# Optimization experiments

Measured on AMD Instinct MI355X. Metric: run time of the kernel, lower is better.

## Reference

```python
import jax, jax.numpy as jnp
import numpy as np

N_ROOMS = 126          # len(building.rooms)
N = 2 + N_ROOMS        # state dim (reset_iv: 2 + n_rooms)
M = 1 + N_ROOMS        # input dim u = [Tout, Q_watts...]
T = 200000             # number of eval times
DT = 30.0              # seconds between eval points
TOUT_DT = 3600.0       # outside-temp table grid spacing (s)
K = 1700               # table length (covers 1000 + T*DT seconds)
LOAD_MAX = 500.0       # physical_loads_scaling: W/m^2 upper bound


def setup_inputs() -> dict:
    key = jax.random.key(0)
    ks = jax.random.split(key, 6)
    # Stable RC-style state matrix: negative diagonal dominates
    A = 1e-5 * jax.random.normal(ks[0], (N, N), dtype=jnp.float32) - 2e-4 * jnp.eye(N, dtype=jnp.float32)
    B = 1e-6 * jax.random.normal(ks[1], (N, M), dtype=jnp.float32)
    loads = jax.random.normal(ks[2], (2, N_ROOMS), dtype=jnp.float32)   # raw params (pre-sigmoid)
    areas = 10.0 + 40.0 * jax.random.uniform(ks[3], (N_ROOMS,), dtype=jnp.float32)  # room areas m^2
    Tout_vals = 10.0 + 5.0 * jax.random.normal(ks[4], (K,), dtype=jnp.float32)      # hourly Tout table
    t_eval = 1000.0 + DT * jnp.arange(T, dtype=jnp.float32)
    iv = 26.0 * jnp.ones((N, 1), dtype=jnp.float32)
    return {"A": A, "B": B, "loads": loads, "areas": areas,
            "Tout_vals": Tout_vals, "t_eval": t_eval, "iv": iv, "action": 1}


def _interp_tout(vals, t):
    # linear interpolation on a uniform grid starting at t=0 (replaces scipy interp1d)
    pos = t / TOUT_DT
    idx = jnp.clip(jnp.floor(pos).astype(jnp.int32), 0, K - 2)
    w = pos - idx.astype(pos.dtype)
    return vals[idx] * (1.0 - w) + vals[idx + 1] * w


def reference(A, B, loads, areas, Tout_vals, t_eval, iv, action):
    t0 = t_eval[0]
    ts = t_eval - t0
    # _build_loads: sigmoid transform + physical scaling
    lp = jax.nn.sigmoid(loads) * LOAD_MAX
    cool_load, gain_load = lp[0], lp[1]
    # f_ode constants: Q_area = -cool*action + gain; Q_watts = proportional_heating
    Q_watts = (-cool_load * action + gain_load) * areas        # [n_rooms]
    b_q = B[:, 1:] @ Q_watts                                   # [N] constant forcing
    b_T = B[:, 0]                                              # [N] Tout coupling
    x0 = iv[:, 0]

    def f(t, x):
        Tout = _interp_tout(Tout_vals, t + t0)
        return A @ x + b_T * Tout + b_q

    # torchdiffeq method='rk4' -> rk4_alt_step_func (3/8 rule)
    def step(x, tt):
        t, tn = tt
        dt = tn - t
        k1 = f(t, x)
        k2 = f(t + dt / 3.0, x + dt * k1 / 3.0)
        k3 = f(t + dt * 2.0 / 3.0, x + dt * (k2 - k1 / 3.0))
        k4 = f(t + dt, x + dt * (k1 - k2 + k3))
        xn = x + dt * (k1 + 3.0 * (k2 + k3) + k4) / 8.0
        return xn, xn

    _, traj = jax.lax.scan(step, x0, (ts[:-1], ts[1:]))
    out = jnp.concatenate([x0[None, :], traj], axis=0)         # [T, N]
    return out[..., None]                                      # [T, N, 1] matching iv shape
```

## Files before the change

kernel.cpp:

```cpp
#include <hip/hip_runtime.h>

#define N 128
#define NR 126
#define MBCOL 127
#define TSTEPS 200000
#define L1 49
#define C1 4096
#define KT 1700

#define OFF_Z     0
#define OFF_S     16384
#define OFF_P     32768
#define OFF_PW2   65536
#define OFF_PW4   81920
#define OFF_PW8   98304
#define OFF_PW16  114688
#define OFF_PW32  131072
#define OFF_Q     147456
#define OFF_WC    180224
#define OFF_ACC   212992
#define OFF_DELTA 737280
#define OFF_B1    753664
#define OFF_B2    1015808
#define OFF_B3    1146880
#define OFF_A16   1212416
#define OFF_C1    1245184
#define OFF_C2    1261568
#define OFF_C3    1269760
#define OFF_A256  1273856
#define OFF_BQ256 1275904
#define OFF_BST16 753664
#define OFF_Q256  786432

typedef float v4f __attribute__((ext_vector_type(4)));
typedef __attribute__((ext_vector_type(8))) short bf16x8;
typedef __attribute__((ext_vector_type(4))) float f32x4;

#define OFF_PEH   65536
#define OFF_PEL   75776

#define LBAR() do { \
  __builtin_amdgcn_sched_barrier(0); \
  asm volatile("s_waitcnt lgkmcnt(0)" ::: "memory"); \
  __builtin_amdgcn_sched_barrier(0); \
  __builtin_amdgcn_s_barrier(); \
  __builtin_amdgcn_sched_barrier(0); \
} while (0)

#define GLD4(dst, p) \
  asm volatile("global_load_dwordx4 %0, %1, off" : "=v"(dst) : "v"(p))
#define PINQ(q) \
  asm volatile("s_waitcnt vmcnt(0)" \
    : "+v"(q[0]),"+v"(q[1]),"+v"(q[2]),"+v"(q[3]), \
      "+v"(q[4]),"+v"(q[5]),"+v"(q[6]),"+v"(q[7]), \
      "+v"(q[8]),"+v"(q[9]),"+v"(q[10]),"+v"(q[11]), \
      "+v"(q[12]),"+v"(q[13]),"+v"(q[14]),"+v"(q[15]))
#define PINQ8(q) \
  asm volatile("s_waitcnt vmcnt(0)" \
    : "+v"(q[0]),"+v"(q[1]),"+v"(q[2]),"+v"(q[3]), \
      "+v"(q[4]),"+v"(q[5]),"+v"(q[6]),"+v"(q[7]))

__device__ __forceinline__ void loadQ16(v4f* qv, const float* pb)
{
  #pragma unroll
  for (int s = 0; s < 16; ++s) GLD4(qv[s], pb + 4*s);
  PINQ(qv);
}

__device__ __forceinline__ void bsplit(float f, unsigned short& h, unsigned short& l)
{
  unsigned int u = __float_as_uint(f);
  unsigned int r = (u + 0x7FFFu + ((u >> 16) & 1u)) >> 16;
  float hf = __uint_as_float(r << 16);
  h = (unsigned short)r;
  float lo = f - hf;
  unsigned int u2 = __float_as_uint(lo);
  unsigned int r2 = (u2 + 0x7FFFu + ((u2 >> 16) & 1u)) >> 16;
  l = (unsigned short)r2;
}

__global__ __launch_bounds__(128) void kPrep(
    const float* __restrict__ A, const float* __restrict__ B,
    const float* __restrict__ loads, const float* __restrict__ areas,
    const float* __restrict__ iv, const int* __restrict__ action,
    float* __restrict__ ws, float* __restrict__ out)
{
  __shared__ float qw[NR];
  __shared__ float ys[4][N];
  __shared__ float qs[4][N];
  int t = threadIdx.x;
  float actf = (float)action[0];
  if (t < NR) {
    float lc = (1.0f / (1.0f + expf(-loads[t]))) * 500.0f;
    float lg = (1.0f / (1.0f + expf(-loads[NR + t]))) * 500.0f;
    qw[t] = (-lc * actf + lg) * areas[t];
  }
  __syncthreads();
  {
    float bq = 0.0f;
    for (int i = 0; i < NR; ++i) bq += B[t * MBCOL + 1 + i] * qw[i];
    ys[0][t] = B[t * MBCOL];
    qs[0][t] = bq;
  }
  __syncthreads();
  for (int s = 1; s < 4; ++s) {
    float ay = 0.0f, aq = 0.0f;
    for (int k = 0; k < N; ++k) {
      float a = A[t * N + k];
      ay += a * ys[s-1][k];
      aq += a * qs[s-1][k];
    }
    ys[s][t] = 30.0f * ay;
    qs[s][t] = 30.0f * aq;
    __syncthreads();
  }
  float vs[5];
  vs[0] = 3.75f * (ys[0][t] + ys[1][t] + ys[2][t]*(1.0f/3.0f) + ys[3][t]*(1.0f/3.0f));
  vs[1] = 3.75f * (3.0f*ys[0][t] + 2.0f*ys[1][t] + ys[2][t]);
  vs[2] = 3.75f * (3.0f*ys[0][t] + ys[1][t]);
  vs[3] = 3.75f * ys[0][t];
  vs[4] = 3.75f * (8.0f*qs[0][t] + 4.0f*qs[1][t] + (4.0f/3.0f)*qs[2][t] + (1.0f/3.0f)*qs[3][t]);
  for (int m = 0; m < 5; ++m) ws[OFF_WC + (m*L1) * N + t] = vs[m];
  for (int i = t; i < N*N/4; i += 128) {
    float4 a = ((const float4*)A)[i];
    a.x *= 30.0f; a.y *= 30.0f; a.z *= 30.0f; a.w *= 30.0f;
    ((float4*)(ws + OFF_Z))[i] = a;
  }
  out[t] = iv[t];
}

__device__ __forceinline__ void mmRowR(const float* __restrict__ Aw,
                                       const float* __restrict__ Bw,
                                       float* __restrict__ Cw,
                                       float* __restrict__ Cw2,
                                       float* __restrict__ sm, int r)
{
  int t = threadIdx.x, c = t & 127, kh = t >> 7;
  const float* Ar = Aw + r*N + kh*64;
  const float* Bc = Bw + (kh*64)*N + c;
  float p0=0.f, p1=0.f, p2=0.f, p3=0.f;
  #pragma unroll 4
  for (int s = 0; s < 64; s += 4) {
    const float4 av = *(const float4*)(Ar + s);
    p0 = fmaf(av.x, Bc[(s+0)*N], p0);
    p1 = fmaf(av.y, Bc[(s+1)*N], p1);
    p2 = fmaf(av.z, Bc[(s+2)*N], p2);
    p3 = fmaf(av.w, Bc[(s+3)*N], p3);
  }
  sm[kh*128 + c] = (p0+p1)+(p2+p3);
  __syncthreads();
  if (kh == 0) {
    float v = sm[c] + sm[128 + c];
    Cw[r*N + c] = v;
    if (Cw2) Cw2[r*N + c] = v;
  }
}

__device__ __forceinline__ void polyRow(float* __restrict__ ws,
                                        float* __restrict__ sm)
{
  int t = threadIdx.x, c = t & 127, kh = t >> 7;
  int r = blockIdx.x;
  const float* Z = ws + OFF_Z;
  const float* S = ws + OFF_S;
  const float* Sr = S + r*N + kh*64;
  float x3=0.f, x4=0.f;
  #pragma unroll 4
  for (int s = 0; s < 64; s += 4) {
    const float4 av = *(const float4*)(Sr + s);
    int k = kh*64 + s;
    x3 = fmaf(av.x, Z[(k+0)*N+c], x3); x3 = fmaf(av.y, Z[(k+1)*N+c], x3);
    x3 = fmaf(av.z, Z[(k+2)*N+c], x3); x3 = fmaf(av.w, Z[(k+3)*N+c], x3);
    x4 = fmaf(av.x, S[(k+0)*N+c], x4); x4 = fmaf(av.y, S[(k+1)*N+c], x4);
    x4 = fmaf(av.z, S[(k+2)*N+c], x4); x4 = fmaf(av.w, S[(k+3)*N+c], x4);
  }
  sm[kh*128 + c] = x3;
  sm[256 + kh*128 + c] = x4;
  __syncthreads();
  if (kh == 0) {
    float a3 = sm[c] + sm[128+c];
    float a4 = sm[256+c] + sm[384+c];
    float pv = (r==c ? 1.0f : 0.0f) + Z[r*N+c] + 0.5f*S[r*N+c]
             + (1.0f/6.0f)*a3 + (1.0f/24.0f)*a4;
    ws[OFF_P + r*N + c] = pv;
  }
}

__device__ __forceinline__ void wUnit(const float* __restrict__ Pw,
                                      float* __restrict__ ws,
                                      int uw, int wbase, int wcount,
                                      float* __restrict__ wbuf )
{
  int t = threadIdx.x;
  int np = 5 * wcount;
  for (int i = t; i < 8*N; i += 256) {
    int pl = i >> 7, k = i & 127;
    int p = uw*8 + pl;
    float v = 0.0f;
    if (p < np) {
      int m = p / wcount, kk = p % wcount;
      v = ws[OFF_WC + (m*L1 + kk)*N + k];
    }
    wbuf[pl*N + k] = v;
  }
  __syncthreads();
  int r = t & 127, pg = t >> 7;
  float acc[4] = {0,0,0,0};
  #pragma unroll 2
  for (int k = 0; k < N; k += 4) {
    const float4 av = *(const float4*)(Pw + r*N + k);
    #pragma unroll
    for (int pi = 0; pi < 4; ++pi) {
      const float4 wv = *(const float4*)(wbuf + (pg*4+pi)*N + k);
      acc[pi] = fmaf(av.x, wv.x, acc[pi]);
      acc[pi] = fmaf(av.y, wv.y, acc[pi]);
      acc[pi] = fmaf(av.z, wv.z, acc[pi]);
      acc[pi] = fmaf(av.w, wv.w, acc[pi]);
    }
  }
  #pragma unroll
  for (int pi = 0; pi < 4; ++pi) {
    int p = uw*8 + pg*4 + pi;
    if (p < np) {
      int m = p / wcount, kk = p % wcount;
      ws[OFF_WC + (m*L1 + wbase + kk)*N + r] = acc[pi];
    }
  }
}

__device__ __forceinline__ void treeUnit(const float* __restrict__ Qm,
                                         const float* __restrict__ src,
                                         float* __restrict__ dst,
                                         int uw, float* __restrict__ wbuf)
{
  int t = threadIdx.x;
  for (int i = t; i < 8*N; i += 256) {
    int pl = i >> 7, k = i & 127;
    wbuf[pl*N + k] = src[(size_t)(2*(uw*8 + pl))*N + k];
  }
  __syncthreads();
  int r = t & 127, pg = t >> 7;
  float acc[4] = {0,0,0,0};
  #pragma unroll 2
  for (int k = 0; k < N; k += 4) {
    const float4 av = *(const float4*)(Qm + r*N + k);
    #pragma unroll
    for (int pi = 0; pi < 4; ++pi) {
      const float4 wv = *(const float4*)(wbuf + (pg*4+pi)*N + k);
      acc[pi] = fmaf(av.x, wv.x, acc[pi]);
      acc[pi] = fmaf(av.y, wv.y, acc[pi]);
      acc[pi] = fmaf(av.z, wv.z, acc[pi]);
      acc[pi] = fmaf(av.w, wv.w, acc[pi]);
    }
  }
  #pragma unroll
  for (int pi = 0; pi < 4; ++pi) {
    int j = uw*8 + pg*4 + pi;
    dst[(size_t)j*N + r] = acc[pi] + src[(size_t)(2*j + 1)*N + r];
  }
}

__global__ __launch_bounds__(256) void kPhase(float* __restrict__ ws, int ph)
{
  __shared__ float sm[1024];
  int b = blockIdx.x;
  if (ph >= 20) {
    int lv = ph - 20;
    const int srcO[8] = {OFF_ACC, OFF_B1, OFF_B2, OFF_B3, OFF_A16, OFF_C1, OFF_C2, OFF_C3};
    const int dstO[8] = {OFF_B1, OFF_B2, OFF_B3, OFF_A16, OFF_C1, OFF_C2, OFF_C3, OFF_A256};
    const int nco[8]  = {2048, 1024, 512, 256, 128, 64, 32, 16};
    const int qO[8]   = {OFF_Q, OFF_S, OFF_P, OFF_PW8, OFF_PW16, OFF_PW32, OFF_Z, OFF_DELTA};
    const int pS[8]   = {OFF_S, OFF_P, OFF_PW8, OFF_PW16, OFF_PW32, OFF_Z, OFF_DELTA, -1};
    const int pD[8]   = {OFF_P, OFF_PW8, OFF_PW16, OFF_PW32, OFF_Z, OFF_DELTA, OFF_Q256, -1};
    int nb = nco[lv] >> 3;
    if (b < nb) treeUnit(ws + qO[lv], ws + srcO[lv], ws + dstO[lv], b, sm);
    else if (pS[lv] >= 0) mmRowR(ws + pS[lv], ws + pS[lv], ws + pD[lv], nullptr, sm, b - nb);
    return;
  }
  if (ph == 1) { mmRowR(ws+OFF_Z, ws+OFF_Z, ws+OFF_S, nullptr, sm, b); return; }
  if (ph == 2) { polyRow(ws, sm); return; }
  if (ph <= 8) {
    int s = ph - 3;
    const int srcOff[6] = {OFF_P, OFF_PW2, OFF_PW4, OFF_PW8, OFF_PW16, OFF_PW32};
    const int dstOff[6] = {OFF_PW2, OFF_PW4, OFF_PW8, OFF_PW16, OFF_PW32, OFF_S};
    if (b < 128) {
      if (s < 5) mmRowR(ws+srcOff[s], ws+srcOff[s], ws+dstOff[s], nullptr, sm, b);
      else       mmRowR(ws+OFF_PW32, ws+OFF_PW16, ws+OFF_S, nullptr, sm, b);
    } else {
      int wbase  = (s < 5) ? (1 << s) : 32;
      int wcount = (s < 5) ? (1 << s) : 17;
      wUnit(ws + srcOff[s], ws, b - 128, wbase, wcount, sm);
    }
    return;
  }
  if (ph == 9) {
    if (b < 128) {
      mmRowR(ws+OFF_S, ws+OFF_P, ws+OFF_Z, ws+OFF_Q, sm, b);
    } else {
      int r = b - 128;
      int tt = threadIdx.x;
      if (tt < 160) {
        float val;
        if (tt < 128)      val = ws[OFF_P + r*N + tt];
        else if (tt < 133) val = ws[OFF_WC + ((tt-128)*L1)*N + r];
        else               val = 0.0f;
        unsigned short h, l2;
        bsplit(val, h, l2);
        ((unsigned short*)(ws + OFF_PEH))[r*160 + tt] = h;
        ((unsigned short*)(ws + OFF_PEL))[r*160 + tt] = l2;
      }
    }
    return;
  }
}

__device__ __forceinline__ void build_table(float* lt, const float* __restrict__ Tout,
                                            int J0, int t, int cnt, int stride)
{
  int tbase = 1470*J0 + 1000;
  for (int s = t; s < cnt; s += stride) {
    float tt = (float)(tbase + 10*s);
    float pos = tt / 3600.0f;
    int idx = (int)pos;
    if (idx > KT-2) idx = KT-2;
    float w = pos - (float)idx;
    lt[s] = Tout[idx]*(1.0f-w) + Tout[idx+1]*w;
  }
}

__global__ __launch_bounds__(256) void k3_acc(const float* __restrict__ Tout,
                                              float* __restrict__ ws)
{
  __shared__ float lt[1184];
  int t = threadIdx.x;
  if (blockIdx.x >= 512) {
    mmRowR(ws+OFF_Z, ws+OFF_Z, ws+OFF_S, nullptr, lt, blockIdx.x - 512);
    return;
  }
  int J0 = blockIdx.x * 8;
  build_table(lt, Tout, J0, t, 1177, 256);
  __syncthreads();
  int r = t & 127, jh = t >> 7;
  float a[4] = {0.0f, 0.0f, 0.0f, 0.0f};
  for (int k = 0; k < L1; ++k) {
    float w0 = ws[OFF_WC + (0*L1+k)*N + r];
    float w1 = ws[OFF_WC + (1*L1+k)*N + r];
    float w2 = ws[OFF_WC + (2*L1+k)*N + r];
    float w3 = ws[OFF_WC + (3*L1+k)*N + r];
    float w4 = ws[OFF_WC + (4*L1+k)*N + r];
    #pragma unroll
    for (int q = 0; q < 4; ++q) {
      int cl = jh*4 + q;
      int soff = 3*(L1*cl + (L1-1) - k);
      a[q] += w0*lt[soff] + w1*lt[soff+1] + w2*lt[soff+2] + w3*lt[soff+3] + w4;
    }
  }
  #pragma unroll
  for (int q = 0; q < 4; ++q)
    ws[OFF_ACC + (size_t)(J0 + jh*4 + q)*N + r] = a[q];
}

__device__ __forceinline__ void mv_step3(const v4f* qv, float* x, float* ps,
                                         int r, int kh, float addv)
{
  const v4f* xp = (const v4f*)(x + kh*64);
  float p0=0.f, p1=0.f, p2=0.f, p3=0.f;
  #pragma unroll
  for (int s = 0; s < 16; s += 4) {
    v4f x0 = xp[s+0], x1 = xp[s+1], x2 = xp[s+2], x3 = xp[s+3];
    p0 = fmaf(qv[s+0][0],x0[0],p0); p0 = fmaf(qv[s+0][1],x0[1],p0);
    p0 = fmaf(qv[s+0][2],x0[2],p0); p0 = fmaf(qv[s+0][3],x0[3],p0);
    p1 = fmaf(qv[s+1][0],x1[0],p1); p1 = fmaf(qv[s+1][1],x1[1],p1);
    p1 = fmaf(qv[s+1][2],x1[2],p1); p1 = fmaf(qv[s+1][3],x1[3],p1);
    p2 = fmaf(qv[s+2][0],x2[0],p2); p2 = fmaf(qv[s+2][1],x2[1],p2);
    p2 = fmaf(qv[s+2][2],x2[2],p2); p2 = fmaf(qv[s+2][3],x2[3],p2);
    p3 = fmaf(qv[s+3][0],x3[0],p3); p3 = fmaf(qv[s+3][1],x3[1],p3);
    p3 = fmaf(qv[s+3][2],x3[2],p3); p3 = fmaf(qv[s+3][3],x3[3],p3);
  }
  ps[kh*128 + r] = (p0+p1)+(p2+p3);
  LBAR();
  if (kh == 0) x[r] = ps[r] + ps[128 + r] + addv;
  LBAR();
}

__global__ __launch_bounds__(256, 2) void k5a_l3(const float* __restrict__ iv,
                                                 float* __restrict__ ws)
{
  __shared__ float x[N];
  __shared__ float ps[256];
  __shared__ float dl[15*N];
  int t = threadIdx.x, r = t & 127, kh = t >> 7;
  v4f qv[16];
  loadQ16(qv, ws + OFF_Q256 + r*N + kh*64);
  for (int i = t; i < 15*N; i += 256) dl[i] = ws[OFF_A256 + i];
  if (t < N) x[t] = iv[t];
  __syncthreads();
  for (int p = 0; p < 16; ++p) {
    if (kh == 0) ws[OFF_BQ256 + p*N + r] = x[r];
    if (p == 15) break;
    mv_step3(qv, x, ps, r, kh, dl[p*N + r]);
  }
}

__global__ __launch_bounds__(256, 2) void k5b_l2(float* __restrict__ ws)
{
  __shared__ float x[N];
  __shared__ float ps[256];
  __shared__ float dl[15*N];
  int t = threadIdx.x, r = t & 127, kh = t >> 7;
  int p = blockIdx.x;
  v4f qv[16];
  loadQ16(qv, ws + OFF_PW16 + r*N + kh*64);
  for (int i = t; i < 15*N; i += 256) dl[i] = ws[OFF_A16 + (size_t)p*15*0 + (size_t)(p*16)*N + i];
  if (t < N) x[t] = ws[OFF_BQ256 + p*N + t];
  __syncthreads();
  for (int i = 0; i < 16; ++i) {
    if (kh == 0) ws[OFF_BST16 + (size_t)(p*16 + i)*N + r] = x[r];
    if (i == 15) break;
    mv_step3(qv, x, ps, r, kh, dl[i*N + r]);
  }
}

__global__ __launch_bounds__(512) void k7_main(const float* __restrict__ Tout,
                                               const float* __restrict__ ws,
                                               float* __restrict__ out)
{
  __shared__ float ltp[3136];
  __shared__ __align__(16) unsigned short XbHi[16][168];
  __shared__ __align__(16) unsigned short XbLo[16][168];
  __shared__ float xf[N];
  __shared__ float psf[512];
  int t = threadIdx.x;
  int m = blockIdx.x;
  int J0 = m * 16;

  for (int e = t; e < 3136; e += 512) {
    int cl = e / 196, rem = e - cl*196;
    int i = rem >> 2, mm = rem & 3;
    float tt = (float)(1000 + 1470*(J0 + cl) + 30*i + 10*mm);
    float pos = tt / 3600.0f;
    int idx = (int)pos;
    if (idx > KT-2) idx = KT-2;
    float w = pos - (float)idx;
    ltp[e] = Tout[idx]*(1.0f-w) + Tout[idx+1]*w;
  }
  for (int e = t; e < 16*40; e += 512) {
    int cn = e / 40, k = 128 + (e - cn*40);
    XbHi[cn][k] = 0; XbLo[cn][k] = 0;
  }
  __syncthreads();
  if (t < 80) {
    int cn = t / 5, mm = t - cn*5;
    float v = (mm < 4) ? ltp[cn*196 + mm] : 1.0f;
    unsigned short h, l2; bsplit(v, h, l2);
    XbHi[cn][128+mm] = h; XbLo[cn][128+mm] = l2;
  }

  int r = t & 127, kq = t >> 7;
  v4f q8[8];
  #pragma unroll
  for (int s = 0; s < 8; ++s) GLD4(q8[s], ws + OFF_Q + r*N + kq*32 + 4*s);
  PINQ8(q8);
  if (t < N) xf[t] = ws[OFF_BST16 + (size_t)m*N + t];
  __syncthreads();
  float nxtA = (t < N) ? ws[OFF_ACC + (size_t)(J0)*N + t] : 0.0f;
  for (int c = 0; c < 16; ++c) {
    if (t < N) {
      unsigned short h, l2; bsplit(xf[t], h, l2);
      XbHi[c][t] = h; XbLo[c][t] = l2;
    }
    if (c == 15) { LBAR(); break; }
    float pp0 = 0.f, pp1 = 0.f;
    const v4f* xp = (const v4f*)(xf + kq*32);
    #pragma unroll
    for (int s = 0; s < 8; s += 2) {
      v4f x0 = xp[s], x1 = xp[s+1];
      pp0 = fmaf(q8[s][0],x0[0],pp0);   pp0 = fmaf(q8[s][1],x0[1],pp0);
      pp0 = fmaf(q8[s][2],x0[2],pp0);   pp0 = fmaf(q8[s][3],x0[3],pp0);
      pp1 = fmaf(q8[s+1][0],x1[0],pp1); pp1 = fmaf(q8[s+1][1],x1[1],pp1);
      pp1 = fmaf(q8[s+1][2],x1[2],pp1); pp1 = fmaf(q8[s+1][3],x1[3],pp1);
    }
    psf[t] = pp0 + pp1;
    LBAR();
    if (t < N) {
      float addv = nxtA;
      nxtA = ws[OFF_ACC + (size_t)(J0 + c + 1)*N + t];
      xf[t] = psf[t] + psf[t+128] + psf[t+256] + psf[t+384] + addv;
    }
    LBAR();
  }

  int l = t & 63, w = t >> 6;
  int la = l & 15, lg = l >> 4;
  int rowA = w*16 + la;
  const unsigned short* peh = (const unsigned short*)(ws + OFF_PEH);
  const unsigned short* pel = (const unsigned short*)(ws + OFF_PEL);
  bf16x8 Ah[5], Al[5];
  #pragma unroll
  for (int kt = 0; kt < 5; ++kt) {
    Ah[kt] = *(const bf16x8*)(peh + rowA*160 + kt*32 + lg*8);
    Al[kt] = *(const bf16x8*)(pel + rowA*160 + kt*32 + lg*8);
  }

  int rowD = w*16 + lg*4;
  int nnB = L1*(J0 + la);
  for (int i = 0; i < L1; ++i) {
    bf16x8 Bh[5], Bl[5];
    #pragma unroll
    for (int kt = 0; kt < 5; ++kt) {
      Bh[kt] = *(const bf16x8*)(&XbHi[la][kt*32 + lg*8]);
      Bl[kt] = *(const bf16x8*)(&XbLo[la][kt*32 + lg*8]);
    }
    f32x4 ahh = {0.f,0.f,0.f,0.f}, ahl = {0.f,0.f,0.f,0.f}, alh = {0.f,0.f,0.f,0.f};
    #pragma unroll
    for (int kt = 0; kt < 5; ++kt) {
      ahh = __builtin_amdgcn_mfma_f32_16x16x32_bf16(Ah[kt], Bh[kt], ahh, 0, 0, 0);
      ahl = __builtin_amdgcn_mfma_f32_16x16x32_bf16(Ah[kt], Bl[kt], ahl, 0, 0, 0);
      alh = __builtin_amdgcn_mfma_f32_16x16x32_bf16(Al[kt], Bh[kt], alh, 0, 0, 0);
    }
    f32x4 y = ahh + ahl + alh;
    int nn = nnB + i + 1;
    if (nn < TSTEPS)
      *(f32x4*)(out + (size_t)nn*N + rowD) = y;
    LBAR();
    unsigned short h0,h1,h2,h3,q0,q1,q2,q3;
    bsplit(y[0],h0,q0); bsplit(y[1],h1,q1); bsplit(y[2],h2,q2); bsplit(y[3],h3,q3);
    unsigned int hA = (unsigned)h0 | ((unsigned)h1<<16);
    unsigned int hB = (unsigned)h2 | ((unsigned)h3<<16);
    unsigned int lA = (unsigned)q0 | ((unsigned)q1<<16);
    unsigned int lB = (unsigned)q2 | ((unsigned)q3<<16);
    *reinterpret_cast<uint2*>(&XbHi[la][rowD]) = make_uint2(hA, hB);
    *reinterpret_cast<uint2*>(&XbLo[la][rowD]) = make_uint2(lA, lB);
    if (t < 64 && i < L1-1) {
      int cn = t >> 2, mm = t & 3;
      float v = ltp[cn*196 + (i+1)*4 + mm];
      unsigned short hh, ll; bsplit(v, hh, ll);
      XbHi[cn][128+mm] = hh; XbLo[cn][128+mm] = ll;
    }
    LBAR();
  }
}

extern "C" void kernel_launch(void* const* d_in, const int* in_sizes, int n_in,
                              void* d_out, int out_size, void* d_ws, size_t ws_size,
                              hipStream_t stream)
{
  const float* A     = (const float*)d_in[0];
  const float* B     = (const float*)d_in[1];
  const float* loads = (const float*)d_in[2];
  const float* areas = (const float*)d_in[3];
  const float* Tout  = (const float*)d_in[4];
  const float* iv    = (const float*)d_in[6];
  const int* action  = (const int*)d_in[7];
  float* out = (float*)d_out;
  float* ws  = (float*)d_ws;

  hipLaunchKernelGGL(kPrep, dim3(1), dim3(128), 0, stream,
                     A, B, loads, areas, iv, action, ws, out);
  const int phGrid[10] = {0, 128, 128, 129, 130, 131, 133, 138, 139, 256};
  for (int ph = 1; ph <= 9; ++ph)
    hipLaunchKernelGGL(kPhase, dim3(phGrid[ph]), dim3(256), 0, stream, ws, ph);
  hipLaunchKernelGGL(k3_acc, dim3(640), dim3(256), 0, stream, Tout, ws);
  const int trGrid[8] = {384, 256, 192, 160, 144, 136, 132, 2};
  for (int lv = 0; lv < 8; ++lv)
    hipLaunchKernelGGL(kPhase, dim3(trGrid[lv]), dim3(256), 0, stream, ws, 20 + lv);
  hipLaunchKernelGGL(k5a_l3, dim3(1),   dim3(256), 0, stream, iv, ws);
  hipLaunchKernelGGL(k5b_l2, dim3(16),  dim3(256), 0, stream, ws);
  hipLaunchKernelGGL(k7_main, dim3(256), dim3(512), 0, stream, Tout, ws, out);
}
```

Baseline: 228.4 us.

## Fold prep and final tree level into other kernels, double-buffer MFMA operand tiles

Removes the separate single-block prep kernel by computing A·A scaled directly from the input A and running the prep work in an extra block of phase 1. The last tree level and the two level-scan kernels are merged into one 16-block kernel, where each block redundantly recomputes the prefix it needs. This cuts the serial launch count by three. The main loop double-buffers the bf16 state tiles in LDS, which removes one barrier per step at the cost of more shared memory and some redundant per-block work in k5ab.

After: 216.3 us. 5.3% less time.

```diff
diff --git a/kernel.cpp b/kernel.cpp
--- a/kernel.cpp
+++ b/kernel.cpp
@@ -27,8 +27,6 @@
 #define OFF_C1    1245184
 #define OFF_C2    1261568
 #define OFF_C3    1269760
-#define OFF_A256  1273856
-#define OFF_BQ256 1275904
 #define OFF_BST16 753664
 #define OFF_Q256  786432
 
@@ -79,61 +77,11 @@
   l = (unsigned short)r2;
 }
 
-__global__ __launch_bounds__(128) void kPrep(
-    const float* __restrict__ A, const float* __restrict__ B,
-    const float* __restrict__ loads, const float* __restrict__ areas,
-    const float* __restrict__ iv, const int* __restrict__ action,
-    float* __restrict__ ws, float* __restrict__ out)
-{
-  __shared__ float qw[NR];
-  __shared__ float ys[4][N];
-  __shared__ float qs[4][N];
-  int t = threadIdx.x;
-  float actf = (float)action[0];
-  if (t < NR) {
-    float lc = (1.0f / (1.0f + expf(-loads[t]))) * 500.0f;
-    float lg = (1.0f / (1.0f + expf(-loads[NR + t]))) * 500.0f;
-    qw[t] = (-lc * actf + lg) * areas[t];
-  }
-  __syncthreads();
-  {
-    float bq = 0.0f;
-    for (int i = 0; i < NR; ++i) bq += B[t * MBCOL + 1 + i] * qw[i];
-    ys[0][t] = B[t * MBCOL];
-    qs[0][t] = bq;
-  }
-  __syncthreads();
-  for (int s = 1; s < 4; ++s) {
-    float ay = 0.0f, aq = 0.0f;
-    for (int k = 0; k < N; ++k) {
-      float a = A[t * N + k];
-      ay += a * ys[s-1][k];
-      aq += a * qs[s-1][k];
-    }
-    ys[s][t] = 30.0f * ay;
-    qs[s][t] = 30.0f * aq;
-    __syncthreads();
-  }
-  float vs[5];
-  vs[0] = 3.75f * (ys[0][t] + ys[1][t] + ys[2][t]*(1.0f/3.0f) + ys[3][t]*(1.0f/3.0f));
-  vs[1] = 3.75f * (3.0f*ys[0][t] + 2.0f*ys[1][t] + ys[2][t]);
-  vs[2] = 3.75f * (3.0f*ys[0][t] + ys[1][t]);
-  vs[3] = 3.75f * ys[0][t];
-  vs[4] = 3.75f * (8.0f*qs[0][t] + 4.0f*qs[1][t] + (4.0f/3.0f)*qs[2][t] + (1.0f/3.0f)*qs[3][t]);
-  for (int m = 0; m < 5; ++m) ws[OFF_WC + (m*L1) * N + t] = vs[m];
-  for (int i = t; i < N*N/4; i += 128) {
-    float4 a = ((const float4*)A)[i];
-    a.x *= 30.0f; a.y *= 30.0f; a.z *= 30.0f; a.w *= 30.0f;
-    ((float4*)(ws + OFF_Z))[i] = a;
-  }
-  out[t] = iv[t];
-}
-
-__device__ __forceinline__ void mmRowR(const float* __restrict__ Aw,
+__device__ __forceinline__ void mmRowS(const float* __restrict__ Aw,
                                        const float* __restrict__ Bw,
                                        float* __restrict__ Cw,
                                        float* __restrict__ Cw2,
-                                       float* __restrict__ sm, int r)
+                                       float* __restrict__ sm, int r, float scale)
 {
   int t = threadIdx.x, c = t & 127, kh = t >> 7;
   const float* Ar = Aw + r*N + kh*64;
@@ -150,18 +98,69 @@
   sm[kh*128 + c] = (p0+p1)+(p2+p3);
   __syncthreads();
   if (kh == 0) {
-    float v = sm[c] + sm[128 + c];
+    float v = (sm[c] + sm[128 + c]) * scale;
     Cw[r*N + c] = v;
     if (Cw2) Cw2[r*N + c] = v;
   }
 }
 
-__device__ __forceinline__ void polyRow(float* __restrict__ ws,
-                                        float* __restrict__ sm)
+#define mmRowR(Aw,Bw,Cw,Cw2,sm,r) mmRowS(Aw,Bw,Cw,Cw2,sm,r,1.0f)
+
+__device__ void prepLite(const float* __restrict__ A, const float* __restrict__ B,
+                         const float* __restrict__ loads, const float* __restrict__ areas,
+                         const float* __restrict__ iv, const int* __restrict__ action,
+                         float* __restrict__ ws, float* __restrict__ out,
+                         float* __restrict__ sm)
+{
+  float* qw = sm;
+  float* ys = sm + 128;
+  float* qs = sm + 640;
+  int t = threadIdx.x;
+  float actf = (float)action[0];
+  if (t < NR) {
+    float lc = (1.0f / (1.0f + expf(-loads[t]))) * 500.0f;
+    float lg = (1.0f / (1.0f + expf(-loads[NR + t]))) * 500.0f;
+    qw[t] = (-lc * actf + lg) * areas[t];
+  }
+  __syncthreads();
+  if (t < N) {
+    float bq = 0.0f;
+    for (int i = 0; i < NR; ++i) bq += B[t * MBCOL + 1 + i] * qw[i];
+    ys[t] = B[t * MBCOL];
+    qs[t] = bq;
+  }
+  __syncthreads();
+  for (int s = 1; s < 4; ++s) {
+    if (t < N) {
+      float ay = 0.0f, aq = 0.0f;
+      for (int k = 0; k < N; ++k) {
+        float a = A[t * N + k];
+        ay += a * ys[(s-1)*N + k];
+        aq += a * qs[(s-1)*N + k];
+      }
+      ys[s*N + t] = 30.0f * ay;
+      qs[s*N + t] = 30.0f * aq;
+    }
+    __syncthreads();
+  }
+  if (t < N) {
+    float y0 = ys[t], y1 = ys[N+t], y2 = ys[2*N+t], y3 = ys[3*N+t];
+    float q0 = qs[t], q1 = qs[N+t], q2 = qs[2*N+t], q3 = qs[3*N+t];
+    ws[OFF_WC + (0*L1)*N + t] = 3.75f * (y0 + y1 + y2*(1.0f/3.0f) + y3*(1.0f/3.0f));
+    ws[OFF_WC + (1*L1)*N + t] = 3.75f * (3.0f*y0 + 2.0f*y1 + y2);
+    ws[OFF_WC + (2*L1)*N + t] = 3.75f * (3.0f*y0 + y1);
+    ws[OFF_WC + (3*L1)*N + t] = 3.75f * y0;
+    ws[OFF_WC + (4*L1)*N + t] = 3.75f * (8.0f*q0 + 4.0f*q1 + (4.0f/3.0f)*q2 + (1.0f/3.0f)*q3);
+    out[t] = iv[t];
+  }
+}
+
+__device__ __forceinline__ void polyRowA(const float* __restrict__ A,
+                                         float* __restrict__ ws,
+                                         float* __restrict__ sm)
 {
   int t = threadIdx.x, c = t & 127, kh = t >> 7;
   int r = blockIdx.x;
-  const float* Z = ws + OFF_Z;
   const float* S = ws + OFF_S;
   const float* Sr = S + r*N + kh*64;
   float x3=0.f, x4=0.f;
@@ -169,8 +168,8 @@
   for (int s = 0; s < 64; s += 4) {
     const float4 av = *(const float4*)(Sr + s);
     int k = kh*64 + s;
-    x3 = fmaf(av.x, Z[(k+0)*N+c], x3); x3 = fmaf(av.y, Z[(k+1)*N+c], x3);
-    x3 = fmaf(av.z, Z[(k+2)*N+c], x3); x3 = fmaf(av.w, Z[(k+3)*N+c], x3);
+    x3 = fmaf(av.x, A[(k+0)*N+c], x3); x3 = fmaf(av.y, A[(k+1)*N+c], x3);
+    x3 = fmaf(av.z, A[(k+2)*N+c], x3); x3 = fmaf(av.w, A[(k+3)*N+c], x3);
     x4 = fmaf(av.x, S[(k+0)*N+c], x4); x4 = fmaf(av.y, S[(k+1)*N+c], x4);
     x4 = fmaf(av.z, S[(k+2)*N+c], x4); x4 = fmaf(av.w, S[(k+3)*N+c], x4);
   }
@@ -178,9 +177,9 @@
   sm[256 + kh*128 + c] = x4;
   __syncthreads();
   if (kh == 0) {
-    float a3 = sm[c] + sm[128+c];
+    float a3 = 30.0f * (sm[c] + sm[128+c]);
     float a4 = sm[256+c] + sm[384+c];
-    float pv = (r==c ? 1.0f : 0.0f) + Z[r*N+c] + 0.5f*S[r*N+c]
+    float pv = (r==c ? 1.0f : 0.0f) + 30.0f*A[r*N+c] + 0.5f*S[r*N+c]
              + (1.0f/6.0f)*a3 + (1.0f/24.0f)*a4;
     ws[OFF_P + r*N + c] = pv;
   }
@@ -260,25 +259,33 @@
   }
 }
 
-__global__ __launch_bounds__(256) void kPhase(float* __restrict__ ws, int ph)
-{
-  __shared__ float sm[1024];
+__global__ __launch_bounds__(256) void kPhase(
+    const float* __restrict__ A, const float* __restrict__ B,
+    const float* __restrict__ loads, const float* __restrict__ areas,
+    const float* __restrict__ iv, const int* __restrict__ action,
+    float* __restrict__ ws, float* __restrict__ out, int ph)
+{
+  __shared__ float sm[1280];
   int b = blockIdx.x;
   if (ph >= 20) {
     int lv = ph - 20;
-    const int srcO[8] = {OFF_ACC, OFF_B1, OFF_B2, OFF_B3, OFF_A16, OFF_C1, OFF_C2, OFF_C3};
-    const int dstO[8] = {OFF_B1, OFF_B2, OFF_B3, OFF_A16, OFF_C1, OFF_C2, OFF_C3, OFF_A256};
-    const int nco[8]  = {2048, 1024, 512, 256, 128, 64, 32, 16};
-    const int qO[8]   = {OFF_Q, OFF_S, OFF_P, OFF_PW8, OFF_PW16, OFF_PW32, OFF_Z, OFF_DELTA};
-    const int pS[8]   = {OFF_S, OFF_P, OFF_PW8, OFF_PW16, OFF_PW32, OFF_Z, OFF_DELTA, -1};
-    const int pD[8]   = {OFF_P, OFF_PW8, OFF_PW16, OFF_PW32, OFF_Z, OFF_DELTA, OFF_Q256, -1};
+    const int srcO[7] = {OFF_ACC, OFF_B1, OFF_B2, OFF_B3, OFF_A16, OFF_C1, OFF_C2};
+    const int dstO[7] = {OFF_B1, OFF_B2, OFF_B3, OFF_A16, OFF_C1, OFF_C2, OFF_C3};
+    const int nco[7]  = {2048, 1024, 512, 256, 128, 64, 32};
+    const int qO[7]   = {OFF_Q, OFF_S, OFF_P, OFF_PW8, OFF_PW16, OFF_PW32, OFF_Z};
+    const int pS[7]   = {OFF_S, OFF_P, OFF_PW8, OFF_PW16, OFF_PW32, OFF_Z, OFF_DELTA};
+    const int pD[7]   = {OFF_P, OFF_PW8, OFF_PW16, OFF_PW32, OFF_Z, OFF_DELTA, OFF_Q256};
     int nb = nco[lv] >> 3;
     if (b < nb) treeUnit(ws + qO[lv], ws + srcO[lv], ws + dstO[lv], b, sm);
-    else if (pS[lv] >= 0) mmRowR(ws + pS[lv], ws + pS[lv], ws + pD[lv], nullptr, sm, b - nb);
+    else mmRowR(ws + pS[lv], ws + pS[lv], ws + pD[lv], nullptr, sm, b - nb);
     return;
   }
-  if (ph == 1) { mmRowR(ws+OFF_Z, ws+OFF_Z, ws+OFF_S, nullptr, sm, b); return; }
-  if (ph == 2) { polyRow(ws, sm); return; }
+  if (ph == 1) {
+    if (b < 128) mmRowS(A, A, ws+OFF_S, nullptr, sm, b, 900.0f);
+    else prepLite(A, B, loads, areas, iv, action, ws, out, sm);
+    return;
+  }
+  if (ph == 2) { polyRowA(A, ws, sm); return; }
   if (ph <= 8) {
     int s = ph - 3;
     const int srcOff[6] = {OFF_P, OFF_PW2, OFF_PW4, OFF_PW8, OFF_PW16, OFF_PW32};
@@ -383,41 +390,52 @@
   LBAR();
 }
 
-__global__ __launch_bounds__(256, 2) void k5a_l3(const float* __restrict__ iv,
-                                                 float* __restrict__ ws)
+__global__ __launch_bounds__(256, 2) void k5ab(const float* __restrict__ iv,
+                                               float* __restrict__ ws)
 {
   __shared__ float x[N];
   __shared__ float ps[256];
-  __shared__ float dl[15*N];
-  int t = threadIdx.x, r = t & 127, kh = t >> 7;
-  v4f qv[16];
-  loadQ16(qv, ws + OFF_Q256 + r*N + kh*64);
-  for (int i = t; i < 15*N; i += 256) dl[i] = ws[OFF_A256 + i];
-  if (t < N) x[t] = iv[t];
-  __syncthreads();
-  for (int p = 0; p < 16; ++p) {
-    if (kh == 0) ws[OFF_BQ256 + p*N + r] = x[r];
-    if (p == 15) break;
-    mv_step3(qv, x, ps, r, kh, dl[p*N + r]);
-  }
-}
-
-__global__ __launch_bounds__(256, 2) void k5b_l2(float* __restrict__ ws)
-{
-  __shared__ float x[N];
-  __shared__ float ps[256];
-  __shared__ float dl[15*N];
+  __shared__ float c3[32*N];
+  __shared__ float aq[15*N];
+  __shared__ float a16d[15*N];
   int t = threadIdx.x, r = t & 127, kh = t >> 7;
   int p = blockIdx.x;
+  for (int i = t; i < 32*N; i += 256) c3[i] = ws[OFF_C3 + i];
+  for (int i = t; i < 15*N; i += 256) a16d[i] = ws[OFF_A16 + (size_t)(p*16)*N + i];
+  if (t < N) x[t] = iv[t];
   v4f qv[16];
+  loadQ16(qv, ws + OFF_DELTA + r*N + kh*64);
+  __syncthreads();
+  for (int q = 0; q < p; ++q) {
+    const v4f* xp = (const v4f*)(c3 + (size_t)(2*q)*N + kh*64);
+    float p0=0.f, p1=0.f, p2=0.f, p3=0.f;
+    #pragma unroll
+    for (int s = 0; s < 16; s += 4) {
+      v4f x0 = xp[s+0], x1 = xp[s+1], x2 = xp[s+2], x3 = xp[s+3];
+      p0 = fmaf(qv[s+0][0],x0[0],p0); p0 = fmaf(qv[s+0][1],x0[1],p0);
+      p0 = fmaf(qv[s+0][2],x0[2],p0); p0 = fmaf(qv[s+0][3],x0[3],p0);
+      p1 = fmaf(qv[s+1][0],x1[0],p1); p1 = fmaf(qv[s+1][1],x1[1],p1);
+      p1 = fmaf(qv[s+1][2],x1[2],p1); p1 = fmaf(qv[s+1][3],x1[3],p1);
+      p2 = fmaf(qv[s+2][0],x2[0],p2); p2 = fmaf(qv[s+2][1],x2[1],p2);
+      p2 = fmaf(qv[s+2][2],x2[2],p2); p2 = fmaf(qv[s+2][3],x2[3],p2);
+      p3 = fmaf(qv[s+3][0],x3[0],p3); p3 = fmaf(qv[s+3][1],x3[1],p3);
+      p3 = fmaf(qv[s+3][2],x3[2],p3); p3 = fmaf(qv[s+3][3],x3[3],p3);
+    }
+    ps[kh*128 + r] = (p0+p1)+(p2+p3);
+    LBAR();
+    if (kh == 0) aq[q*N + r] = ps[r] + ps[128 + r] + c3[(size_t)(2*q+1)*N + r];
+    LBAR();
+  }
+  loadQ16(qv, ws + OFF_Q256 + r*N + kh*64);
+  __syncthreads();
+  for (int q = 0; q < p; ++q)
+    mv_step3(qv, x, ps, r, kh, aq[q*N + r]);
   loadQ16(qv, ws + OFF_PW16 + r*N + kh*64);
-  for (int i = t; i < 15*N; i += 256) dl[i] = ws[OFF_A16 + (size_t)p*15*0 + (size_t)(p*16)*N + i];
-  if (t < N) x[t] = ws[OFF_BQ256 + p*N + t];
   __syncthreads();
   for (int i = 0; i < 16; ++i) {
     if (kh == 0) ws[OFF_BST16 + (size_t)(p*16 + i)*N + r] = x[r];
     if (i == 15) break;
-    mv_step3(qv, x, ps, r, kh, dl[i*N + r]);
+    mv_step3(qv, x, ps, r, kh, a16d[i*N + r]);
   }
 }
 
@@ -426,8 +444,8 @@
                                                float* __restrict__ out)
 {
   __shared__ float ltp[3136];
-  __shared__ __align__(16) unsigned short XbHi[16][168];
-  __shared__ __align__(16) unsigned short XbLo[16][168];
+  __shared__ __align__(16) unsigned short XbHi[2][16][168];
+  __shared__ __align__(16) unsigned short XbLo[2][16][168];
   __shared__ float xf[N];
   __shared__ float psf[512];
   int t = threadIdx.x;
@@ -444,16 +462,17 @@
     float w = pos - (float)idx;
     ltp[e] = Tout[idx]*(1.0f-w) + Tout[idx+1]*w;
   }
-  for (int e = t; e < 16*40; e += 512) {
-    int cn = e / 40, k = 128 + (e - cn*40);
-    XbHi[cn][k] = 0; XbLo[cn][k] = 0;
+  for (int e = t; e < 2*16*40; e += 512) {
+    int bu = e / 640, rem = e - bu*640;
+    int cn = rem / 40, k = 128 + (rem - cn*40);
+    XbHi[bu][cn][k] = 0; XbLo[bu][cn][k] = 0;
   }
   __syncthreads();
   if (t < 80) {
     int cn = t / 5, mm = t - cn*5;
     float v = (mm < 4) ? ltp[cn*196 + mm] : 1.0f;
     unsigned short h, l2; bsplit(v, h, l2);
-    XbHi[cn][128+mm] = h; XbLo[cn][128+mm] = l2;
+    XbHi[0][cn][128+mm] = h; XbLo[0][cn][128+mm] = l2;
   }
 
   int r = t & 127, kq = t >> 7;
@@ -467,7 +486,7 @@
   for (int c = 0; c < 16; ++c) {
     if (t < N) {
       unsigned short h, l2; bsplit(xf[t], h, l2);
-      XbHi[c][t] = h; XbLo[c][t] = l2;
+      XbHi[0][c][t] = h; XbLo[0][c][t] = l2;
     }
     if (c == 15) { LBAR(); break; }
     float pp0 = 0.f, pp1 = 0.f;
@@ -505,11 +524,12 @@
   int rowD = w*16 + lg*4;
   int nnB = L1*(J0 + la);
   for (int i = 0; i < L1; ++i) {
+    int cur = i & 1, nxt = cur ^ 1;
     bf16x8 Bh[5], Bl[5];
     #pragma unroll
     for (int kt = 0; kt < 5; ++kt) {
-      Bh[kt] = *(const bf16x8*)(&XbHi[la][kt*32 + lg*8]);
-      Bl[kt] = *(const bf16x8*)(&XbLo[la][kt*32 + lg*8]);
+      Bh[kt] = *(const bf16x8*)(&XbHi[cur][la][kt*32 + lg*8]);
+      Bl[kt] = *(const bf16x8*)(&XbLo[cur][la][kt*32 + lg*8]);
     }
     f32x4 ahh = {0.f,0.f,0.f,0.f}, ahl = {0.f,0.f,0.f,0.f}, alh = {0.f,0.f,0.f,0.f};
     #pragma unroll
@@ -522,20 +542,19 @@
     int nn = nnB + i + 1;
     if (nn < TSTEPS)
       *(f32x4*)(out + (size_t)nn*N + rowD) = y;
-    LBAR();
     unsigned short h0,h1,h2,h3,q0,q1,q2,q3;
     bsplit(y[0],h0,q0); bsplit(y[1],h1,q1); bsplit(y[2],h2,q2); bsplit(y[3],h3,q3);
     unsigned int hA = (unsigned)h0 | ((unsigned)h1<<16);
     unsigned int hB = (unsigned)h2 | ((unsigned)h3<<16);
     unsigned int lA = (unsigned)q0 | ((unsigned)q1<<16);
     unsigned int lB = (unsigned)q2 | ((unsigned)q3<<16);
-    *reinterpret_cast<uint2*>(&XbHi[la][rowD]) = make_uint2(hA, hB);
-    *reinterpret_cast<uint2*>(&XbLo[la][rowD]) = make_uint2(lA, lB);
-    if (t < 64 && i < L1-1) {
-      int cn = t >> 2, mm = t & 3;
-      float v = ltp[cn*196 + (i+1)*4 + mm];
+    *reinterpret_cast<uint2*>(&XbHi[nxt][la][rowD]) = make_uint2(hA, hB);
+    *reinterpret_cast<uint2*>(&XbLo[nxt][la][rowD]) = make_uint2(lA, lB);
+    if (t < 80 && i < L1-1) {
+      int cn = t / 5, mm = t - cn*5;
+      float v = (mm < 4) ? ltp[cn*196 + (i+1)*4 + mm] : 1.0f;
       unsigned short hh, ll; bsplit(v, hh, ll);
-      XbHi[cn][128+mm] = hh; XbLo[cn][128+mm] = ll;
+      XbHi[nxt][cn][128+mm] = hh; XbLo[nxt][cn][128+mm] = ll;
     }
     LBAR();
   }
@@ -555,16 +574,15 @@
   float* out = (float*)d_out;
   float* ws  = (float*)d_ws;
 
-  hipLaunchKernelGGL(kPrep, dim3(1), dim3(128), 0, stream,
-                     A, B, loads, areas, iv, action, ws, out);
-  const int phGrid[10] = {0, 128, 128, 129, 130, 131, 133, 138, 139, 256};
+  const int phGrid[10] = {0, 129, 128, 129, 130, 131, 133, 138, 139, 256};
   for (int ph = 1; ph <= 9; ++ph)
-    hipLaunchKernelGGL(kPhase, dim3(phGrid[ph]), dim3(256), 0, stream, ws, ph);
+    hipLaunchKernelGGL(kPhase, dim3(phGrid[ph]), dim3(256), 0, stream,
+                       A, B, loads, areas, iv, action, ws, out, ph);
   hipLaunchKernelGGL(k3_acc, dim3(640), dim3(256), 0, stream, Tout, ws);
-  const int trGrid[8] = {384, 256, 192, 160, 144, 136, 132, 2};
-  for (int lv = 0; lv < 8; ++lv)
-    hipLaunchKernelGGL(kPhase, dim3(trGrid[lv]), dim3(256), 0, stream, ws, 20 + lv);
-  hipLaunchKernelGGL(k5a_l3, dim3(1),   dim3(256), 0, stream, iv, ws);
-  hipLaunchKernelGGL(k5b_l2, dim3(16),  dim3(256), 0, stream, ws);
+  const int trGrid[7] = {384, 256, 192, 160, 144, 136, 132};
+  for (int lv = 0; lv < 7; ++lv)
+    hipLaunchKernelGGL(kPhase, dim3(trGrid[lv]), dim3(256), 0, stream,
+                       A, B, loads, areas, iv, action, ws, out, 20 + lv);
+  hipLaunchKernelGGL(k5ab,   dim3(16),  dim3(256), 0, stream, iv, ws);
   hipLaunchKernelGGL(k7_main, dim3(256), dim3(512), 0, stream, Tout, ws, out);
 }
```
